# Kernel optimization log

Measured on AMD Instinct MI355X. Metric: run time of the kernel, lower is better.

The kernel has to match this reference:

```python
import jax, jax.numpy as jnp
import numpy as np

D_MODEL = 256
N_LEVELS = 4
N_HEADS = 8
N_POINTS = 4
LEN_Q = 1024
LEN_X = 256
SHAPES_NP = np.array([[100, 100], [50, 50], [25, 25], [13, 13]], dtype=np.int32)
LEN_IN = int((SHAPES_NP[:, 0] * SHAPES_NP[:, 1]).sum())  # 13294


def setup_inputs() -> dict:
    key = jax.random.key(0)
    ks = jax.random.split(key, 10)
    s = 0.02
    lvl_start = np.concatenate([[0], np.cumsum(SHAPES_NP[:, 0] * SHAPES_NP[:, 1])[:-1]]).astype(np.int32)
    return {
        "query": jax.random.normal(ks[0], (1, LEN_Q, D_MODEL), jnp.float32),
        "reference_points": jax.random.uniform(ks[1], (1, LEN_Q, N_LEVELS, 2), jnp.float32),
        "input_flatten": jax.random.normal(ks[2], (1, LEN_IN, D_MODEL), jnp.float32),
        "input_spatial_shapes": jnp.asarray(SHAPES_NP, jnp.int32),
        "add_keys": jax.random.normal(ks[3], (1, LEN_X, D_MODEL), jnp.float32),
        "input_level_start_index": jnp.asarray(lvl_start, jnp.int32),
        "W_off": jax.random.normal(ks[4], (N_HEADS * N_LEVELS * N_POINTS * 2, D_MODEL), jnp.float32) * s,
        "b_off": jax.random.normal(ks[5], (N_HEADS * N_LEVELS * N_POINTS * 2,), jnp.float32),
        "W_attn": jax.random.normal(ks[6], (N_HEADS * (N_LEVELS + 1), D_MODEL, D_MODEL), jnp.float32) * s,
        "W_val": jax.random.normal(ks[7], (2 * N_HEADS, D_MODEL, D_MODEL), jnp.float32) * s,
        "b_val": jax.random.normal(ks[8], (2 * N_HEADS, D_MODEL), jnp.float32) * s,
        "W_mix": jax.random.normal(ks[9], (D_MODEL, N_HEADS + 1), jnp.float32) * s,
    }


def reference(query, reference_points, input_flatten, input_spatial_shapes, add_keys,
              input_level_start_index, W_off, b_off, W_attn, W_val, b_val, W_mix):
    N, Lq, C = query.shape
    H, L, P = N_HEADS, N_LEVELS, N_POINTS

    # sampling offsets: (N, Lq, H, L, P, 2)
    off = (query @ W_off.T + b_off).reshape(N, Lq, H, L, P, 2)
    iss_f = input_spatial_shapes.astype(jnp.float32)          # (L, 2) = (H_l, W_l)
    wh = iss_f[:, ::-1]                                        # (W_l, H_l)
    loc = reference_points[:, :, None, :, None, :] + off / wh[None, None, None, :, None, :]

    # get_keys: clamp, quantize to int index (matches torch .int() trunc, values >= 0)
    loc = jnp.clip(loc, 0.0, 0.999)
    idx = (loc * iss_f[None, None, None, :, None, :]).astype(jnp.int32)
    h_l = input_spatial_shapes[:, 0]                           # (L,)
    flat_idx = (idx[..., 0] + idx[..., 1] * h_l[None, None, None, :, None]
                + input_level_start_index[None, None, None, :, None])   # (N, Lq, H, L, P)
    keys = input_flatten[0][flat_idx[0]]                       # (Lq, H, L, P, C)
    keys = jnp.transpose(keys, (1, 2, 3, 0, 4))                # (H, L, P, Lq, C)

    q = query.reshape(Lq, C)
    head_w = jax.nn.softmax(W_mix.T, axis=0)                   # (H+1, C), softmax over heads
    result = q * head_w[-1][None]
    addk = add_keys.reshape(-1, C)                             # (Lx, C)

    for h in range(H):
        attn = []
        for lvl in range(L):
            simil = W_attn[h * L + lvl]
            # faithful to torch: (C, P*Lq) row-major reshaped to (P, Lq, C)
            ki = (simil @ keys[h, lvl].reshape(-1, C).T).reshape(P, Lq, C)
            attn.append((ki * q[None]).sum(-1))                # (P, Lq)
        simil = W_attn[h * L + L]
        ki = addk @ simil.T                                    # (Lx, C)
        attn.append(ki @ q.T)                                  # (Lx, Lq)
        attn = jax.nn.softmax(jnp.concatenate(attn, axis=0), axis=0)  # (L*P+Lx, Lq)

        vals = (keys[h].reshape(-1, C) @ W_val[2 * h].T + b_val[2 * h]).reshape(L * P, Lq, C)
        v2 = addk @ W_val[2 * h + 1].T + b_val[2 * h + 1]      # (Lx, C)
        vals = jnp.concatenate([vals, jnp.broadcast_to(v2[:, None], (v2.shape[0], Lq, C))], axis=0)
        result = result + (attn[:, :, None] * vals).sum(0) * head_w[h][None]

    return result[None]
```

## Files before the change

### kernel.cpp

```cpp
#include <hip/hip_runtime.h>

typedef unsigned short ushort_t;
typedef __attribute__((ext_vector_type(8))) short bh8;
typedef __attribute__((ext_vector_type(4))) float f4;
typedef __attribute__((ext_vector_type(4))) unsigned int u4;

__device__ __forceinline__ ushort_t f2bf(float f) {
  unsigned u = __float_as_uint(f);
  return (ushort_t)((u + 0x7FFFu + ((u >> 16) & 1u)) >> 16);
}
__device__ __forceinline__ float bf2f(ushort_t v) {
  return __uint_as_float(((unsigned)v) << 16);
}

template <typename OutT>
__device__ __forceinline__ void gemm_abt_core(
    char* smem,
    const ushort_t* __restrict__ A, const ushort_t* __restrict__ B,
    OutT* __restrict__ C, int ldA, int ldB, int ldC, int K, int m0, int n0)
{
  ushort_t* As = (ushort_t*)smem;
  ushort_t* Bs = (ushort_t*)(smem + 10240);
  int t = threadIdx.x;
  int lane = t & 63, w = t >> 6;
  int quad = lane >> 4, l15 = lane & 15;
  int wm = w >> 1, wn = w & 1;
  f4 acc[4][4];
  #pragma unroll
  for (int mi = 0; mi < 4; ++mi)
    #pragma unroll
    for (int ni = 0; ni < 4; ++ni) acc[mi][ni] = (f4)0.f;
  int row = t >> 1, kh = (t & 1) * 16;
  const ushort_t* pa = A + (m0 + row) * ldA + kh;
  const ushort_t* pb = B + (n0 + row) * ldB + kh;
  u4 va0 = *(const u4*)(pa);     u4 va1 = *(const u4*)(pa + 8);
  u4 vb0 = *(const u4*)(pb);     u4 vb1 = *(const u4*)(pb + 8);
  for (int k0 = 0; k0 < K; k0 += 32) {
    if (k0) __syncthreads();
    {
      u4* da = (u4*)(As + row * 40 + kh); da[0] = va0; da[1] = va1;
      u4* db = (u4*)(Bs + row * 40 + kh); db[0] = vb0; db[1] = vb1;
    }
    if (k0 + 32 < K) {
      va0 = *(const u4*)(pa + k0 + 32); va1 = *(const u4*)(pa + k0 + 40);
      vb0 = *(const u4*)(pb + k0 + 32); vb1 = *(const u4*)(pb + k0 + 40);
    }
    __syncthreads();
    bh8 af[4], bfv[4];
    #pragma unroll
    for (int mi = 0; mi < 4; ++mi)
      af[mi] = *(bh8*)(As + (wm * 64 + mi * 16 + l15) * 40 + quad * 8);
    #pragma unroll
    for (int ni = 0; ni < 4; ++ni)
      bfv[ni] = *(bh8*)(Bs + (wn * 64 + ni * 16 + l15) * 40 + quad * 8);
    #pragma unroll
    for (int mi = 0; mi < 4; ++mi)
      #pragma unroll
      for (int ni = 0; ni < 4; ++ni)
        acc[mi][ni] = __builtin_amdgcn_mfma_f32_16x16x32_bf16(af[mi], bfv[ni], acc[mi][ni], 0, 0, 0);
  }
  #pragma unroll
  for (int mi = 0; mi < 4; ++mi)
    #pragma unroll
    for (int ni = 0; ni < 4; ++ni)
      #pragma unroll
      for (int r = 0; r < 4; ++r) {
        int mg = m0 + wm * 64 + mi * 16 + quad * 4 + r;
        int ng = n0 + wn * 64 + ni * 16 + l15;
        if constexpr (sizeof(OutT) == 4) C[mg * ldC + ng] = acc[mi][ni][r];
        else C[mg * ldC + ng] = (OutT)f2bf(acc[mi][ni][r]);
      }
}

__device__ __forceinline__ void gemm_abt_f32in(
    char* smem,
    const float* __restrict__ A, const float* __restrict__ B,
    ushort_t* __restrict__ C, int ldA, int ldB, int ldC, int K, int m0, int n0)
{
  ushort_t* As = (ushort_t*)smem;
  ushort_t* Bs = (ushort_t*)(smem + 10240);
  int t = threadIdx.x;
  int lane = t & 63, w = t >> 6;
  int quad = lane >> 4, l15 = lane & 15;
  int wm = w >> 1, wn = w & 1;
  f4 acc[4][4];
  #pragma unroll
  for (int mi = 0; mi < 4; ++mi)
    #pragma unroll
    for (int ni = 0; ni < 4; ++ni) acc[mi][ni] = (f4)0.f;
  int row = t >> 1, kh = (t & 1) * 16;
  const float* pa = A + (m0 + row) * ldA + kh;
  const float* pb = B + (n0 + row) * ldB + kh;
  float4 fa[4], fb[4];
  #pragma unroll
  for (int i = 0; i < 4; ++i) {
    fa[i] = *(const float4*)(pa + i * 4);
    fb[i] = *(const float4*)(pb + i * 4);
  }
  for (int k0 = 0; k0 < K; k0 += 32) {
    if (k0) __syncthreads();
    {
      ushort_t* da = As + row * 40 + kh;
      ushort_t* db = Bs + row * 40 + kh;
      #pragma unroll
      for (int i = 0; i < 4; ++i) {
        ushort4 oa; oa.x = f2bf(fa[i].x); oa.y = f2bf(fa[i].y);
        oa.z = f2bf(fa[i].z); oa.w = f2bf(fa[i].w);
        *(ushort4*)(da + i * 4) = oa;
        ushort4 ob; ob.x = f2bf(fb[i].x); ob.y = f2bf(fb[i].y);
        ob.z = f2bf(fb[i].z); ob.w = f2bf(fb[i].w);
        *(ushort4*)(db + i * 4) = ob;
      }
    }
    if (k0 + 32 < K) {
      #pragma unroll
      for (int i = 0; i < 4; ++i) {
        fa[i] = *(const float4*)(pa + k0 + 32 + i * 4);
        fb[i] = *(const float4*)(pb + k0 + 32 + i * 4);
      }
    }
    __syncthreads();
    bh8 af[4], bfv[4];
    #pragma unroll
    for (int mi = 0; mi < 4; ++mi)
      af[mi] = *(bh8*)(As + (wm * 64 + mi * 16 + l15) * 40 + quad * 8);
    #pragma unroll
    for (int ni = 0; ni < 4; ++ni)
      bfv[ni] = *(bh8*)(Bs + (wn * 64 + ni * 16 + l15) * 40 + quad * 8);
    #pragma unroll
    for (int mi = 0; mi < 4; ++mi)
      #pragma unroll
      for (int ni = 0; ni < 4; ++ni)
        acc[mi][ni] = __builtin_amdgcn_mfma_f32_16x16x32_bf16(af[mi], bfv[ni], acc[mi][ni], 0, 0, 0);
  }
  #pragma unroll
  for (int mi = 0; mi < 4; ++mi)
    #pragma unroll
    for (int ni = 0; ni < 4; ++ni)
      #pragma unroll
      for (int r = 0; r < 4; ++r) {
        int mg = m0 + wm * 64 + mi * 16 + quad * 4 + r;
        int ng = n0 + wn * 64 + ni * 16 + l15;
        C[mg * ldC + ng] = (ushort_t)f2bf(acc[mi][ni][r]);
      }
}

__global__ __launch_bounds__(256) void k_fused_cast_off(
    const float* __restrict__ q, const float* __restrict__ xin,
    const float* __restrict__ addk, const float* __restrict__ Wval,
    const float* __restrict__ Wattn, ushort_t* __restrict__ arena,
    const float* __restrict__ Woff, const float* __restrict__ boff,
    const float* __restrict__ refpts, const int* __restrict__ shapes,
    const int* __restrict__ lvlst, int* __restrict__ fidx,
    ushort_t* __restrict__ tmp)
{
  __shared__ __align__(16) char smem[20480];
  if (blockIdx.x >= 96) {
    const int total4 = 1719168;
    for (int i = (blockIdx.x - 96) * 256 + threadIdx.x; i < total4; i += 1952 * 256) {
      const float* src; ushort_t* dst; int e;
      if (i < 65536)        { src = q    + i * 4;            dst = arena + i * 4; }
      else if (i < 916352)  { e = i - 65536;  src = xin  + e * 4; dst = arena + 262144  + e * 4; }
      else if (i < 932736)  { e = i - 916352; src = addk + e * 4; dst = arena + 3665408 + e * 4; }
      else if (i < 1194880) {
        e = i - 932736; int el = e * 4;
        int h = el >> 17, r = el & 131071;
        int c = r >> 9, k = r & 511;
        src = Wval + (2 * h + (k >> 8)) * 65536 + c * 256 + (k & 255);
        dst = arena + 3730944 + el;
      }
      else {
        e = i - 1194880;
        src = Wattn + e * 4;
        dst = arena + 6352384 + e * 4;
      }
      float4 v = *(const float4*)src;
      ushort4 o; o.x = f2bf(v.x); o.y = f2bf(v.y); o.z = f2bf(v.z); o.w = f2bf(v.w);
      *(ushort4*)dst = o;
    }
  } else if (blockIdx.x >= 64) {
    int e = blockIdx.x - 64;
    int h = e >> 2, rem = e & 3, my = rem >> 1, nx = rem & 1;
    gemm_abt_f32in(smem, addk, Wattn + (h * 4 + 4) * 65536, tmp + h * 65536,
                   256, 256, 256, 256, my * 128, nx * 128);
  } else {
    float(*As)[65] = (float(*)[65])smem;
    float(*Bs)[65] = (float(*)[65])(smem + 16 * 65 * 4);
    int e = blockIdx.x;
    int nx = e & 3, my = e >> 2;
    int m0 = my * 64, n0 = nx * 64;
    int t = threadIdx.x;
    int tm = t & 15, tn = t >> 4;
    int lr = t >> 4, lc = t & 15;
    float acc[4][4] = {};
    float qa[4], wb[4];
    #pragma unroll
    for (int i = 0; i < 4; ++i) {
      int r = lr + i * 16;
      qa[i] = q[(m0 + r) * 256 + lc];
      wb[i] = Woff[(n0 + r) * 256 + lc];
    }
    for (int k0 = 0; k0 < 256; k0 += 16) {
      if (k0) __syncthreads();
      #pragma unroll
      for (int i = 0; i < 4; ++i) {
        int r = lr + i * 16;
        As[lc][r] = qa[i];
        Bs[lc][r] = wb[i];
      }
      if (k0 + 16 < 256) {
        #pragma unroll
        for (int i = 0; i < 4; ++i) {
          int r = lr + i * 16;
          qa[i] = q[(m0 + r) * 256 + k0 + 16 + lc];
          wb[i] = Woff[(n0 + r) * 256 + k0 + 16 + lc];
        }
      }
      __syncthreads();
      #pragma unroll
      for (int k = 0; k < 16; ++k) {
        float a[4], b[4];
        #pragma unroll
        for (int i = 0; i < 4; ++i) a[i] = As[k][tm * 4 + i];
        #pragma unroll
        for (int j = 0; j < 4; ++j) b[j] = Bs[k][tn * 4 + j];
        #pragma unroll
        for (int i = 0; i < 4; ++i)
          #pragma unroll
          for (int j = 0; j < 4; ++j) acc[i][j] += a[i] * b[j];
      }
    }
    #pragma unroll
    for (int i = 0; i < 4; ++i) {
      int b = m0 + tm * 4 + i;
      #pragma unroll
      for (int jp = 0; jp < 2; ++jp) {
        int tt = ((n0 + tn * 4) >> 1) + jp;
        int l = (tt >> 2) & 3;
        float off0 = acc[i][jp * 2]     + boff[2 * tt];
        float off1 = acc[i][jp * 2 + 1] + boff[2 * tt + 1];
        int Hi = shapes[2 * l], Wi = shapes[2 * l + 1];
        float Hf = (float)Hi, Wf = (float)Wi;
        float r0 = refpts[b * 8 + 2 * l], r1 = refpts[b * 8 + 2 * l + 1];
        float l0 = fminf(fmaxf(r0 + off0 / Wf, 0.f), 0.999f);
        float l1 = fminf(fmaxf(r1 + off1 / Hf, 0.f), 0.999f);
        int i0 = (int)(l0 * Hf);
        int i1 = (int)(l1 * Wf);
        fidx[b * 128 + tt] = i0 + i1 * Hi + lvlst[l];
      }
    }
  }
}

__device__ __forceinline__ void attn_mfma_body(
    char* smemc,
    const ushort_t* __restrict__ qbf, const ushort_t* __restrict__ xbf,
    const ushort_t* __restrict__ Wlvl, const int* __restrict__ fidx,
    float* __restrict__ attnP, int bx)
{
  unsigned* Bs = (unsigned*)smemc;
  ushort_t* As = (ushort_t*)(smemc + 8704);
  int* fis = (int*)(smemc + 17920);
  float* Nlds = (float*)smemc;

  int h = bx >> 8, l = (bx >> 6) & 3, g = bx & 63;
  int ch = g & 3, g2 = g >> 2;
  int p = g2 >> 2, tg = g2 & 3;
  int c0 = ch * 64;
  int t = threadIdx.x;
  int lane = t & 63, w = t >> 6;
  int quad = lane >> 4, l15 = lane & 15;
  int qcol = p * 4 + tg;
  fis[t] = fidx[(tg * 256 + t) * 128 + h * 16 + l * 4 + p];
  __syncthreads();
  f4 acc[4];
  #pragma unroll
  for (int mi = 0; mi < 4; ++mi) acc[mi] = (f4)0.f;

  int cl = t & 63, sg = t >> 6;
  int uu = t >> 2, jj0 = (t & 3) * 16;
  const ushort_t* qrow = qbf + (uu * 16 + qcol) * 256 + jj0;

  unsigned vv[16];
  u4 a0, a1;
  #pragma unroll
  for (int rr = 0; rr < 16; ++rr)
    vv[rr] = xbf[fis[sg * 16 + rr] * 256 + c0 + cl];
  { const u4* src = (const u4*)qrow; a0 = src[0]; a1 = src[1]; }

  #pragma unroll
  for (int jt = 0; jt < 4; ++jt) {
    if (jt) __syncthreads();
    #pragma unroll
    for (int i = 0; i < 4; ++i) {
      uint2 w2; w2.x = vv[i * 4] | (vv[i * 4 + 1] << 16);
      w2.y = vv[i * 4 + 2] | (vv[i * 4 + 3] << 16);
      *(uint2*)&Bs[cl * 34 + sg * 8 + i * 2] = w2;
    }
    { u4* dst = (u4*)(As + uu * 72 + jj0); dst[0] = a0; dst[1] = a1; }
    if (jt < 3) {
      #pragma unroll
      for (int rr = 0; rr < 16; ++rr)
        vv[rr] = xbf[fis[(jt + 1) * 64 + sg * 16 + rr] * 256 + c0 + cl];
      const u4* src = (const u4*)(qrow + (jt + 1) * 64);
      a0 = src[0]; a1 = src[1];
    }
    __syncthreads();
    #pragma unroll
    for (int ks = 0; ks < 2; ++ks) {
      bh8 af[4], bfv;
      #pragma unroll
      for (int mi = 0; mi < 4; ++mi)
        af[mi] = *(bh8*)(As + (mi * 16 + l15) * 72 + ks * 32 + quad * 8);
      {
        const unsigned* bp = &Bs[(w * 16 + l15) * 34 + ks * 16 + quad * 4];
        uint2 b0 = *(const uint2*)bp;
        uint2 b1 = *(const uint2*)(bp + 2);
        u4 bb; bb.x = b0.x; bb.y = b0.y; bb.z = b1.x; bb.w = b1.y;
        bfv = __builtin_bit_cast(bh8, bb);
      }
      #pragma unroll
      for (int mi = 0; mi < 4; ++mi)
        acc[mi] = __builtin_amdgcn_mfma_f32_16x16x32_bf16(af[mi], bfv, acc[mi], 0, 0, 0);
    }
  }
  __syncthreads();
  #pragma unroll
  for (int mi = 0; mi < 4; ++mi)
    *(f4*)&Nlds[(w * 16 + l15) * 68 + mi * 16 + quad * 4] = acc[mi];
  __syncthreads();
  {
    int a = t >> 6, u = t & 63;
    const ushort_t* Wr = Wlvl + (h * 4 + l) * 65536 + (a * 64 + u) * 256 + c0;
    float s = 0.f;
    #pragma unroll
    for (int cc = 0; cc < 8; ++cc) {
      u4 wv = *(const u4*)(Wr + cc * 8);
      int cb = cc * 8;
      s += __uint_as_float(wv.x << 16)         * Nlds[(cb + 0) * 68 + u];
      s += __uint_as_float(wv.x & 0xffff0000u) * Nlds[(cb + 1) * 68 + u];
      s += __uint_as_float(wv.y << 16)         * Nlds[(cb + 2) * 68 + u];
      s += __uint_as_float(wv.y & 0xffff0000u) * Nlds[(cb + 3) * 68 + u];
      s += __uint_as_float(wv.z << 16)         * Nlds[(cb + 4) * 68 + u];
      s += __uint_as_float(wv.z & 0xffff0000u) * Nlds[(cb + 5) * 68 + u];
      s += __uint_as_float(wv.w << 16)         * Nlds[(cb + 6) * 68 + u];
      s += __uint_as_float(wv.w & 0xffff0000u) * Nlds[(cb + 7) * 68 + u];
    }
    attnP[ch * 131072 + (h * 16 + l * 4 + a) * 1024 + u * 16 + qcol] = s;
  }
}

__global__ __launch_bounds__(256) void k_fused_attn(
    const ushort_t* __restrict__ qbf, const ushort_t* __restrict__ xbf,
    const ushort_t* __restrict__ Wlvl, const int* __restrict__ fidx,
    float* __restrict__ attnP,
    const ushort_t* __restrict__ tmp, float* __restrict__ attn)
{
  __shared__ __align__(16) char smem[20480];
  int bx = blockIdx.x;
  if (bx >= 128) {
    attn_mfma_body(smem, qbf, xbf, Wlvl, fidx, attnP, bx - 128);
  } else {
    int e = bx;
    int h = e >> 4, rem = e & 15, my = rem >> 3, nx = rem & 7;
    gemm_abt_core<float>(smem, tmp + h * 65536, qbf, attn + h * 278528 + 16384,
                         256, 256, 1024, 256, my * 128, nx * 128);
  }
}

__global__ __launch_bounds__(256) void k_softmax(
    float* __restrict__ attn, const float* __restrict__ attnP,
    ushort_t* __restrict__ attn2bf, float* __restrict__ s1, float* __restrict__ s2)
{
  __shared__ float red[16][17];
  int h = blockIdx.y;
  int bl = threadIdx.x & 15;
  int b = blockIdx.x * 16 + bl;
  int rg = threadIdx.x >> 4;
  const int R0 = rg * 17;
  float* col = attn + h * 278528 + b;
  float v[17];
  float m = -1e30f;
  #pragma unroll
  for (int i = 0; i < 17; ++i) {
    int r = R0 + i;
    float x;
    if (r < 16) {
      int idx = (h * 16 + r) * 1024 + b;
      x = attnP[idx] + attnP[131072 + idx] + attnP[262144 + idx] + attnP[393216 + idx];
    } else {
      x = col[r * 1024];
    }
    v[i] = x;
    m = fmaxf(m, x);
  }
  red[rg][bl] = m;
  __syncthreads();
  #pragma unroll
  for (int j = 0; j < 16; ++j) m = fmaxf(m, red[j][bl]);
  float sum = 0.f;
  #pragma unroll
  for (int i = 0; i < 17; ++i) { v[i] = expf(v[i] - m); sum += v[i]; }
  __syncthreads();
  red[rg][bl] = sum;
  __syncthreads();
  float tot = 0.f;
  #pragma unroll
  for (int j = 0; j < 16; ++j) tot += red[j][bl];
  float inv = 1.f / tot;
  #pragma unroll
  for (int i = 0; i < 17; ++i) {
    int r = R0 + i;
    float x = v[i] * inv;
    if (r < 16) col[r * 1024] = x;
    else attn2bf[h * 262144 + (r - 16) * 1024 + b] = f2bf(x);
  }
  if (rg == 0) {
    float sa = 0.f;
    #pragma unroll
    for (int i = 0; i < 16; ++i) sa += v[i];
    float sn = sa * inv;
    s1[h * 1024 + b] = sn;
    s2[h * 1024 + b] = 1.f - sn;
  }
}

__global__ __launch_bounds__(256) void k_fused_kbar_tn(
    const ushort_t* __restrict__ xbf, const float* __restrict__ attn,
    const int* __restrict__ fidx, const ushort_t* __restrict__ attn2,
    const ushort_t* __restrict__ addk, ushort_t* __restrict__ kabar)
{
  __shared__ __align__(16) unsigned Asu[128 * 20];
  __shared__ __align__(16) unsigned Bsu[128 * 20];
  if (blockIdx.x >= 128) {
    int bb = blockIdx.x - 128;
    int h = bb >> 7, b0 = (bb & 127) * 8;
    int t = threadIdx.x;
    int qi = t >> 5, oct = t & 31;
    int b = b0 + qi;
    float aw[16]; int rowv[16];
    #pragma unroll
    for (int r = 0; r < 16; ++r) {
      aw[r]   = attn[(h * 272 + r) * 1024 + b];
      rowv[r] = fidx[b * 128 + h * 16 + r];
    }
    u4 va[8], vb[8];
    #pragma unroll
    for (int r = 0; r < 8; ++r) va[r] = *(const u4*)(xbf + rowv[r] * 256 + oct * 8);
    #pragma unroll
    for (int r = 0; r < 8; ++r) vb[r] = *(const u4*)(xbf + rowv[8 + r] * 256 + oct * 8);
    float sacc[8] = {};
    #pragma unroll
    for (int r = 0; r < 8; ++r) {
      u4 v = va[r]; float w = aw[r];
      sacc[0] += w * __uint_as_float(v.x << 16);
      sacc[1] += w * __uint_as_float(v.x & 0xffff0000u);
      sacc[2] += w * __uint_as_float(v.y << 16);
      sacc[3] += w * __uint_as_float(v.y & 0xffff0000u);
      sacc[4] += w * __uint_as_float(v.z << 16);
      sacc[5] += w * __uint_as_float(v.z & 0xffff0000u);
      sacc[6] += w * __uint_as_float(v.w << 16);
      sacc[7] += w * __uint_as_float(v.w & 0xffff0000u);
    }
    #pragma unroll
    for (int r = 0; r < 8; ++r) {
      u4 v = vb[r]; float w = aw[8 + r];
      sacc[0] += w * __uint_as_float(v.x << 16);
      sacc[1] += w * __uint_as_float(v.x & 0xffff0000u);
      sacc[2] += w * __uint_as_float(v.y << 16);
      sacc[3] += w * __uint_as_float(v.y & 0xffff0000u);
      sacc[4] += w * __uint_as_float(v.z << 16);
      sacc[5] += w * __uint_as_float(v.z & 0xffff0000u);
      sacc[6] += w * __uint_as_float(v.w << 16);
      sacc[7] += w * __uint_as_float(v.w & 0xffff0000u);
    }
    u4 o;
    o.x = (unsigned)f2bf(sacc[0]) | ((unsigned)f2bf(sacc[1]) << 16);
    o.y = (unsigned)f2bf(sacc[2]) | ((unsigned)f2bf(sacc[3]) << 16);
    o.z = (unsigned)f2bf(sacc[4]) | ((unsigned)f2bf(sacc[5]) << 16);
    o.w = (unsigned)f2bf(sacc[6]) | ((unsigned)f2bf(sacc[7]) << 16);
    *(u4*)(kabar + (h * 1024 + b) * 512 + oct * 8) = o;
  } else {
    int e = blockIdx.x;
    int h = e >> 4, rem = e & 15, my = rem >> 1, nx = rem & 1;
    const ushort_t* A = attn2 + h * 262144;
    const ushort_t* B = addk;
    ushort_t* C = kabar + h * 524288;
    int m0 = my * 128, n0 = nx * 128;
    int t = threadIdx.x;
    int lane = t & 63, w = t >> 6;
    int quad = lane >> 4, l15 = lane & 15;
    int wm = w >> 1, wn = w & 1;
    f4 acc[4][4];
    #pragma unroll
    for (int mi = 0; mi < 4; ++mi)
      #pragma unroll
      for (int ni = 0; ni < 4; ++ni) acc[mi][ni] = (f4)0.f;
    int col = t & 127, half = t >> 7;
    unsigned pa[8], pb[8];
    #pragma unroll
    for (int i = 0; i < 4; ++i) {
      int kpp = half * 4 + i, kk = kpp * 4;
      unsigned x0 = A[(kk + 0) * 1024 + m0 + col], x1 = A[(kk + 1) * 1024 + m0 + col];
      unsigned x2 = A[(kk + 2) * 1024 + m0 + col], x3 = A[(kk + 3) * 1024 + m0 + col];
      pa[i * 2] = x0 | (x1 << 16); pa[i * 2 + 1] = x2 | (x3 << 16);
      unsigned y0 = B[(kk + 0) * 256 + n0 + col], y1 = B[(kk + 1) * 256 + n0 + col];
      unsigned y2 = B[(kk + 2) * 256 + n0 + col], y3 = B[(kk + 3) * 256 + n0 + col];
      pb[i * 2] = y0 | (y1 << 16); pb[i * 2 + 1] = y2 | (y3 << 16);
    }
    for (int k0 = 0; k0 < 256; k0 += 32) {
      if (k0) __syncthreads();
      #pragma unroll
      for (int i = 0; i < 4; ++i) {
        int kpp = half * 4 + i;
        uint2 va; va.x = pa[i * 2]; va.y = pa[i * 2 + 1];
        *(uint2*)&Asu[col * 20 + kpp * 2] = va;
        uint2 vbv; vbv.x = pb[i * 2]; vbv.y = pb[i * 2 + 1];
        *(uint2*)&Bsu[col * 20 + kpp * 2] = vbv;
      }
      if (k0 + 32 < 256) {
        #pragma unroll
        for (int i = 0; i < 4; ++i) {
          int kpp = half * 4 + i, kk = k0 + 32 + kpp * 4;
          unsigned x0 = A[(kk + 0) * 1024 + m0 + col], x1 = A[(kk + 1) * 1024 + m0 + col];
          unsigned x2 = A[(kk + 2) * 1024 + m0 + col], x3 = A[(kk + 3) * 1024 + m0 + col];
          pa[i * 2] = x0 | (x1 << 16); pa[i * 2 + 1] = x2 | (x3 << 16);
          unsigned y0 = B[(kk + 0) * 256 + n0 + col], y1 = B[(kk + 1) * 256 + n0 + col];
          unsigned y2 = B[(kk + 2) * 256 + n0 + col], y3 = B[(kk + 3) * 256 + n0 + col];
          pb[i * 2] = y0 | (y1 << 16); pb[i * 2 + 1] = y2 | (y3 << 16);
        }
      }
      __syncthreads();
      bh8 af[4], bfv[4];
      #pragma unroll
      for (int mi = 0; mi < 4; ++mi)
        af[mi] = *(bh8*)((const ushort_t*)Asu + (wm * 64 + mi * 16 + l15) * 40 + quad * 8);
      #pragma unroll
      for (int ni = 0; ni < 4; ++ni)
        bfv[ni] = *(bh8*)((const ushort_t*)Bsu + (wn * 64 + ni * 16 + l15) * 40 + quad * 8);
      #pragma unroll
      for (int mi = 0; mi < 4; ++mi)
        #pragma unroll
        for (int ni = 0; ni < 4; ++ni)
          acc[mi][ni] = __builtin_amdgcn_mfma_f32_16x16x32_bf16(af[mi], bfv[ni], acc[mi][ni], 0, 0, 0);
    }
    #pragma unroll
    for (int mi = 0; mi < 4; ++mi)
      #pragma unroll
      for (int ni = 0; ni < 4; ++ni)
        #pragma unroll
        for (int r = 0; r < 4; ++r) {
          int mg = m0 + wm * 64 + mi * 16 + quad * 4 + r;
          int ng = n0 + wn * 64 + ni * 16 + l15;
          C[mg * 512 + 256 + ng] = f2bf(acc[mi][ni][r]);
        }
  }
}

__global__ __launch_bounds__(256) void gemm_val_k(
    const ushort_t* __restrict__ kabar, const ushort_t* __restrict__ Wcat,
    float* __restrict__ Y)
{
  __shared__ __align__(16) char smem[20480];
  int h = blockIdx.z;
  gemm_abt_core<float>(smem, kabar + h * 524288, Wcat + h * 131072, Y + h * 262144,
                       512, 512, 256, 512, blockIdx.y * 128, blockIdx.x * 128);
}

__global__ __launch_bounds__(256) void k_combine(
    const float* __restrict__ q, const float* __restrict__ Wmix,
    const float* __restrict__ Y,
    const float* __restrict__ s1, const float* __restrict__ s2,
    const float* __restrict__ bval, float* __restrict__ out)
{
  int b = blockIdx.x, c = threadIdx.x;
  float w[9];
  float m = -1e30f;
  #pragma unroll
  for (int j = 0; j < 9; ++j) { w[j] = Wmix[c * 9 + j]; m = fmaxf(m, w[j]); }
  float tot = 0.f;
  #pragma unroll
  for (int j = 0; j < 9; ++j) { w[j] = expf(w[j] - m); tot += w[j]; }
  float inv = 1.f / tot;
  float res = q[b * 256 + c] * w[8] * inv;
  #pragma unroll
  for (int hh = 0; hh < 8; ++hh) {
    float y = Y[(hh * 1024 + b) * 256 + c]
            + s1[hh * 1024 + b] * bval[(2 * hh) * 256 + c]
            + s2[hh * 1024 + b] * bval[(2 * hh + 1) * 256 + c];
    res += w[hh] * inv * y;
  }
  out[b * 256 + c] = res;
}

extern "C" void kernel_launch(void* const* d_in, const int* in_sizes, int n_in,
                              void* d_out, int out_size, void* d_ws, size_t ws_size,
                              hipStream_t stream) {
  (void)in_sizes; (void)n_in; (void)out_size; (void)ws_size;
  const float* q      = (const float*)d_in[0];
  const float* refpts = (const float*)d_in[1];
  const float* xin    = (const float*)d_in[2];
  const int*   shapes = (const int*)d_in[3];
  const float* addk   = (const float*)d_in[4];
  const int*   lvlst  = (const int*)d_in[5];
  const float* Woff   = (const float*)d_in[6];
  const float* boff   = (const float*)d_in[7];
  const float* Wattn  = (const float*)d_in[8];
  const float* Wval   = (const float*)d_in[9];
  const float* bval   = (const float*)d_in[10];
  const float* Wmix   = (const float*)d_in[11];
  float* out = (float*)d_out;
  float* ws  = (float*)d_ws;

  int*   fidx    = (int*)ws;
  float* s1      = ws + 393216;
  float* s2      = ws + 401408;
  float* attn    = ws + 409600;
  float* Y       = ws + 409600;
  ushort_t* arena = (ushort_t*)(ws + 2637824);
  ushort_t* q_bf     = arena;
  ushort_t* xin_bf   = arena + 262144;
  ushort_t* addk_bf  = arena + 3665408;
  ushort_t* Wcat_bf  = arena + 3730944;
  ushort_t* Wlvl_bf  = arena + 6352384;
  ushort_t* tmp_bf   = arena + 8449536;
  ushort_t* attn2_bf = arena + 8973824;
  ushort_t* kabar_bf = arena + 11070976;
  float* attnP = (float*)(arena + 15265280);

  k_fused_cast_off<<<2048, 256, 0, stream>>>(q, xin, addk, Wval, Wattn, arena,
                                             Woff, boff, refpts, shapes, lvlst,
                                             fidx, tmp_bf);
  k_fused_attn<<<2176, 256, 0, stream>>>(q_bf, xin_bf, Wlvl_bf, fidx, attnP,
                                         tmp_bf, attn);
  k_softmax<<<dim3(64, 8), 256, 0, stream>>>(attn, attnP, attn2_bf, s1, s2);
  k_fused_kbar_tn<<<1152, 256, 0, stream>>>(xin_bf, attn, fidx, attn2_bf,
                                            addk_bf, kabar_bf);
  gemm_val_k<<<dim3(2, 8, 8), 256, 0, stream>>>(kabar_bf, Wcat_bf, Y);
  k_combine<<<1024, 256, 0, stream>>>(q, Wmix, Y, s1, s2, bval, out);
}
```

Baseline: 178.5 us.

## Double-buffer LDS in gathered attention MFMA and split GEMM tiles to 128x64

The gathered-key attention body now uses two LDS buffers, so the gather and staging for the next 64-row tile overlap the MFMAs on the current one, with one barrier per step instead of two. The add-key GEMM part of the fused kernel moves from 128x128 to 128x64 tiles, doubling its block count to spread work over more CUs. Shared memory per block grows from 20 KB to 36 KB and launch bounds request 4 blocks per SM, which may limit occupancy or increase register pressure.

Result: no change. 178.0 us (-0.3%).

```diff
diff --git a/kernel.cpp b/kernel.cpp
--- a/kernel.cpp
+++ b/kernel.cpp
@@ -69,6 +69,64 @@
         int ng = n0 + wn * 64 + ni * 16 + l15;
         if constexpr (sizeof(OutT) == 4) C[mg * ldC + ng] = acc[mi][ni][r];
         else C[mg * ldC + ng] = (OutT)f2bf(acc[mi][ni][r]);
+      }
+}
+
+__device__ __forceinline__ void gemm_abt_12864(
+    char* smem,
+    const ushort_t* __restrict__ A, const ushort_t* __restrict__ B,
+    float* __restrict__ C, int ldA, int ldB, int ldC, int K, int m0, int n0)
+{
+  ushort_t* As = (ushort_t*)smem;
+  ushort_t* Bs = (ushort_t*)(smem + 10240);
+  int t = threadIdx.x;
+  int lane = t & 63, w = t >> 6;
+  int quad = lane >> 4, l15 = lane & 15;
+  int wm = w >> 1, wn = w & 1;
+  f4 acc[4][2];
+  #pragma unroll
+  for (int mi = 0; mi < 4; ++mi)
+    #pragma unroll
+    for (int ni = 0; ni < 2; ++ni) acc[mi][ni] = (f4)0.f;
+  int rowA = t >> 1, khA = (t & 1) * 16;
+  int rowB = t >> 2, khB = (t & 3) * 8;
+  const ushort_t* pa = A + (m0 + rowA) * ldA + khA;
+  const ushort_t* pb = B + (n0 + rowB) * ldB + khB;
+  u4 va0 = *(const u4*)(pa); u4 va1 = *(const u4*)(pa + 8);
+  u4 vb0 = *(const u4*)(pb);
+  for (int k0 = 0; k0 < K; k0 += 32) {
+    if (k0) __syncthreads();
+    {
+      u4* da = (u4*)(As + rowA * 40 + khA); da[0] = va0; da[1] = va1;
+      u4* db = (u4*)(Bs + rowB * 40 + khB); db[0] = vb0;
+    }
+    if (k0 + 32 < K) {
+      va0 = *(const u4*)(pa + k0 + 32); va1 = *(const u4*)(pa + k0 + 40);
+      vb0 = *(const u4*)(pb + k0 + 32);
+    }
+    __syncthreads();
+    bh8 af[4], bf2[2];
+    #pragma unroll
+    for (int mi = 0; mi < 4; ++mi)
+      af[mi] = *(bh8*)(As + (wm * 64 + mi * 16 + l15) * 40 + quad * 8);
+    #pragma unroll
+    for (int ni = 0; ni < 2; ++ni)
+      bf2[ni] = *(bh8*)(Bs + (wn * 32 + ni * 16 + l15) * 40 + quad * 8);
+    #pragma unroll
+    for (int mi = 0; mi < 4; ++mi)
+      #pragma unroll
+      for (int ni = 0; ni < 2; ++ni)
+        acc[mi][ni] = __builtin_amdgcn_mfma_f32_16x16x32_bf16(af[mi], bf2[ni], acc[mi][ni], 0, 0, 0);
+  }
+  #pragma unroll
+  for (int mi = 0; mi < 4; ++mi)
+    #pragma unroll
+    for (int ni = 0; ni < 2; ++ni)
+      #pragma unroll
+      for (int r = 0; r < 4; ++r) {
+        int mg = m0 + wm * 64 + mi * 16 + quad * 4 + r;
+        int ng = n0 + wn * 32 + ni * 16 + l15;
+        C[mg * ldC + ng] = acc[mi][ni][r];
       }
 }
 
@@ -258,9 +316,11 @@
     const ushort_t* __restrict__ Wlvl, const int* __restrict__ fidx,
     float* __restrict__ attnP, int bx)
 {
-  unsigned* Bs = (unsigned*)smemc;
-  ushort_t* As = (ushort_t*)(smemc + 8704);
-  int* fis = (int*)(smemc + 17920);
+  unsigned* Bs0 = (unsigned*)smemc;
+  unsigned* Bs1 = (unsigned*)(smemc + 8704);
+  ushort_t* As0 = (ushort_t*)(smemc + 17408);
+  ushort_t* As1 = (ushort_t*)(smemc + 26624);
+  int* fis = (int*)(smemc + 35840);
   float* Nlds = (float*)smemc;
 
   int h = bx >> 8, l = (bx >> 6) & 3, g = bx & 63;
@@ -287,33 +347,49 @@
   for (int rr = 0; rr < 16; ++rr)
     vv[rr] = xbf[fis[sg * 16 + rr] * 256 + c0 + cl];
   { const u4* src = (const u4*)qrow; a0 = src[0]; a1 = src[1]; }
+  #pragma unroll
+  for (int i = 0; i < 4; ++i) {
+    uint2 w2; w2.x = vv[i * 4] | (vv[i * 4 + 1] << 16);
+    w2.y = vv[i * 4 + 2] | (vv[i * 4 + 3] << 16);
+    *(uint2*)&Bs0[cl * 34 + sg * 8 + i * 2] = w2;
+  }
+  { u4* dst = (u4*)(As0 + uu * 72 + jj0); dst[0] = a0; dst[1] = a1; }
+  #pragma unroll
+  for (int rr = 0; rr < 16; ++rr)
+    vv[rr] = xbf[fis[64 + sg * 16 + rr] * 256 + c0 + cl];
+  { const u4* src = (const u4*)(qrow + 64); a0 = src[0]; a1 = src[1]; }
+  __syncthreads();
 
   #pragma unroll
   for (int jt = 0; jt < 4; ++jt) {
-    if (jt) __syncthreads();
-    #pragma unroll
-    for (int i = 0; i < 4; ++i) {
-      uint2 w2; w2.x = vv[i * 4] | (vv[i * 4 + 1] << 16);
-      w2.y = vv[i * 4 + 2] | (vv[i * 4 + 3] << 16);
-      *(uint2*)&Bs[cl * 34 + sg * 8 + i * 2] = w2;
-    }
-    { u4* dst = (u4*)(As + uu * 72 + jj0); dst[0] = a0; dst[1] = a1; }
+    unsigned* Bc = (jt & 1) ? Bs1 : Bs0;
+    ushort_t* Ac = (jt & 1) ? As1 : As0;
     if (jt < 3) {
-      #pragma unroll
-      for (int rr = 0; rr < 16; ++rr)
-        vv[rr] = xbf[fis[(jt + 1) * 64 + sg * 16 + rr] * 256 + c0 + cl];
-      const u4* src = (const u4*)(qrow + (jt + 1) * 64);
-      a0 = src[0]; a1 = src[1];
-    }
-    __syncthreads();
+      unsigned* Bn = (jt & 1) ? Bs0 : Bs1;
+      ushort_t* An = (jt & 1) ? As0 : As1;
+      #pragma unroll
+      for (int i = 0; i < 4; ++i) {
+        uint2 w2; w2.x = vv[i * 4] | (vv[i * 4 + 1] << 16);
+        w2.y = vv[i * 4 + 2] | (vv[i * 4 + 3] << 16);
+        *(uint2*)&Bn[cl * 34 + sg * 8 + i * 2] = w2;
+      }
+      { u4* dst = (u4*)(An + uu * 72 + jj0); dst[0] = a0; dst[1] = a1; }
+      if (jt < 2) {
+        #pragma unroll
+        for (int rr = 0; rr < 16; ++rr)
+          vv[rr] = xbf[fis[(jt + 2) * 64 + sg * 16 + rr] * 256 + c0 + cl];
+        const u4* src = (const u4*)(qrow + (jt + 2) * 64);
+        a0 = src[0]; a1 = src[1];
+      }
+    }
     #pragma unroll
     for (int ks = 0; ks < 2; ++ks) {
       bh8 af[4], bfv;
       #pragma unroll
       for (int mi = 0; mi < 4; ++mi)
-        af[mi] = *(bh8*)(As + (mi * 16 + l15) * 72 + ks * 32 + quad * 8);
+        af[mi] = *(bh8*)(Ac + (mi * 16 + l15) * 72 + ks * 32 + quad * 8);
       {
-        const unsigned* bp = &Bs[(w * 16 + l15) * 34 + ks * 16 + quad * 4];
+        const unsigned* bp = &Bc[(w * 16 + l15) * 34 + ks * 16 + quad * 4];
         uint2 b0 = *(const uint2*)bp;
         uint2 b1 = *(const uint2*)(bp + 2);
         u4 bb; bb.x = b0.x; bb.y = b0.y; bb.z = b1.x; bb.w = b1.y;
@@ -323,6 +399,7 @@
       for (int mi = 0; mi < 4; ++mi)
         acc[mi] = __builtin_amdgcn_mfma_f32_16x16x32_bf16(af[mi], bfv, acc[mi], 0, 0, 0);
     }
+    if (jt < 3) __syncthreads();
   }
   __syncthreads();
   #pragma unroll
@@ -350,21 +427,21 @@
   }
 }
 
-__global__ __launch_bounds__(256) void k_fused_attn(
+__global__ __launch_bounds__(256, 4) void k_fused_attn(
     const ushort_t* __restrict__ qbf, const ushort_t* __restrict__ xbf,
     const ushort_t* __restrict__ Wlvl, const int* __restrict__ fidx,
     float* __restrict__ attnP,
     const ushort_t* __restrict__ tmp, float* __restrict__ attn)
 {
-  __shared__ __align__(16) char smem[20480];
+  __shared__ __align__(16) char smem[36864];
   int bx = blockIdx.x;
-  if (bx >= 128) {
-    attn_mfma_body(smem, qbf, xbf, Wlvl, fidx, attnP, bx - 128);
+  if (bx >= 256) {
+    attn_mfma_body(smem, qbf, xbf, Wlvl, fidx, attnP, bx - 256);
   } else {
     int e = bx;
-    int h = e >> 4, rem = e & 15, my = rem >> 3, nx = rem & 7;
-    gemm_abt_core<float>(smem, tmp + h * 65536, qbf, attn + h * 278528 + 16384,
-                         256, 256, 1024, 256, my * 128, nx * 128);
+    int h = e >> 5, rem = e & 31, my = rem >> 4, nx = rem & 15;
+    gemm_abt_12864(smem, tmp + h * 65536, qbf, attn + h * 278528 + 16384,
+                   256, 256, 1024, 256, my * 128, nx * 64);
   }
 }
 
@@ -631,7 +708,7 @@
   k_fused_cast_off<<<2048, 256, 0, stream>>>(q, xin, addk, Wval, Wattn, arena,
                                              Woff, boff, refpts, shapes, lvlst,
                                              fidx, tmp_bf);
-  k_fused_attn<<<2176, 256, 0, stream>>>(q_bf, xin_bf, Wlvl_bf, fidx, attnP,
+  k_fused_attn<<<2304, 256, 0, stream>>>(q_bf, xin_bf, Wlvl_bf, fidx, attnP,
                                          tmp_bf, attn);
   k_softmax<<<dim3(64, 8), 256, 0, stream>>>(attn, attnP, attn2_bf, s1, s2);
   k_fused_kbar_tn<<<1152, 256, 0, stream>>>(xin_bf, attn, fidx, attn2_bf,
```
